# Kernel tuning notes

Measured on AMD Instinct MI355X. Metric: run time of the kernel, lower is better.

The kernel has to match this reference:

```python
import jax, jax.numpy as jnp
import numpy as np

D_MODEL = 1024
NUM_HEAD = 16
HEAD_DIM = D_MODEL // NUM_HEAD  # 64


def setup_inputs() -> dict:
    key = jax.random.key(0)
    ks = jax.random.split(key, 9)
    B, S = 2, 2048
    s = 0.02
    return {
        "x": jax.random.normal(ks[0], (B, S, D_MODEL), dtype=jnp.float32),
        "Wq": jax.random.normal(ks[1], (D_MODEL, D_MODEL), dtype=jnp.float32) * s,
        "bq": jax.random.normal(ks[2], (D_MODEL,), dtype=jnp.float32) * s,
        "Wk": jax.random.normal(ks[3], (D_MODEL, D_MODEL), dtype=jnp.float32) * s,
        "bk": jax.random.normal(ks[4], (D_MODEL,), dtype=jnp.float32) * s,
        "Wv": jax.random.normal(ks[5], (D_MODEL, D_MODEL), dtype=jnp.float32) * s,
        "bv": jax.random.normal(ks[6], (D_MODEL,), dtype=jnp.float32) * s,
        "Wo": jax.random.normal(ks[7], (D_MODEL, D_MODEL), dtype=jnp.float32) * s,
        "bo": jax.random.normal(ks[8], (D_MODEL,), dtype=jnp.float32) * s,
    }


def _split_head(t):
    # [B,S,D] -> [B,H,S,hd]
    B, S, _ = t.shape
    return t.reshape(B, S, NUM_HEAD, HEAD_DIM).transpose(0, 2, 1, 3)


def reference(x, Wq, bq, Wk, bk, Wv, bv, Wo, bo):
    B, S, D = x.shape
    q = _split_head(x @ Wq.T + bq)  # [B,H,S,hd]
    k = _split_head(x @ Wk.T + bk)
    v = _split_head(x @ Wv.T + bv)
    scale = 1.0 / jnp.sqrt(jnp.asarray(HEAD_DIM, dtype=x.dtype))
    scores = jnp.einsum("bhqd,bhkd->bhqk", q, k) * scale  # [B,H,S,S]
    attn = jax.nn.softmax(scores, axis=-1)
    out = jnp.einsum("bhqk,bhkd->bhqd", attn, v)  # [B,H,S,hd]
    out = out.transpose(0, 2, 1, 3).reshape(B, S, D)
    return out @ Wo.T + bo
```

## Files before the change

### kernel.cpp

```cpp
#include <hip/hip_runtime.h>
#include <cstdint>


typedef unsigned short ush;
typedef __bf16 bf16x8 __attribute__((ext_vector_type(8)));
typedef float f32x4 __attribute__((ext_vector_type(4)));
typedef ush u16x8 __attribute__((ext_vector_type(8)));
typedef ush u16x4 __attribute__((ext_vector_type(4)));
typedef unsigned int u32x4 __attribute__((ext_vector_type(4)));

__device__ __forceinline__ ush f2bf(float f) {
  unsigned int u = __float_as_uint(f);
  u += 0x7fffu + ((u >> 16) & 1u);
  return (ush)(u >> 16);
}

__device__ __forceinline__ unsigned int pack2bf_ru(float a, float b) {
  unsigned int ua = __float_as_uint(a) + 0x8000u;
  unsigned int ub = __float_as_uint(b) + 0x8000u;
  return __builtin_amdgcn_perm(ub, ua, 0x07060302u);
}

__device__ __forceinline__ bf16x8 bc8(u16x8 v) {
  return __builtin_bit_cast(bf16x8, v);
}

__device__ __forceinline__ void async16(const void* g, void* l) {
  __builtin_amdgcn_global_load_lds(
      (const __attribute__((address_space(1))) unsigned int*)(uintptr_t)g,
      (__attribute__((address_space(3))) unsigned int*)(uintptr_t)l, 16, 0, 0);
}

__global__ __launch_bounds__(256) void convert_kernel(
    const float* __restrict__ x, const float* __restrict__ Wq,
    const float* __restrict__ Wk, const float* __restrict__ Wv,
    const float* __restrict__ Wo,
    ush* __restrict__ xb, ush* __restrict__ Wqb, ush* __restrict__ Wkb,
    ush* __restrict__ Wvb, ush* __restrict__ Wob)
{
  int tid = blockIdx.x * 256 + threadIdx.x;
  int base = tid * 4;
  const float* src; ush* dst; int idx;
  if (base < 4194304) { src = x; dst = xb; idx = base; }
  else {
    int r = base - 4194304;
    int seg = r >> 20;
    idx = r & 1048575;
    src = seg == 0 ? Wq : seg == 1 ? Wk : seg == 2 ? Wv : Wo;
    dst = seg == 0 ? Wqb : seg == 1 ? Wkb : seg == 2 ? Wvb : Wob;
  }
  float4 f = *(const float4*)(src + idx);
  u16x4 u = { f2bf(f.x), f2bf(f.y), f2bf(f.z), f2bf(f.w) };
  *(u16x4*)(dst + idx) = u;
}

__device__ __forceinline__ void gemm128_core(
    const ush* __restrict__ gA, const ush* __restrict__ gB,
    int m0, int n0, ush* lA, ush* lB, f32x4 (&acc)[4][4])
{
  const int t = threadIdx.x, w = t >> 6, lane = t & 63;
  const int l15 = lane & 15, quad = lane >> 4;
  const int wm = (w >> 1) * 64, wn = (w & 1) * 64;
#pragma unroll
  for (int i = 0; i < 4; ++i)
#pragma unroll
    for (int j = 0; j < 4; ++j) acc[i][j] = (f32x4){0.f, 0.f, 0.f, 0.f};

  for (int kt = 0; kt < 1024; kt += 64) {
#pragma unroll
    for (int i = 0; i < 4; ++i) {
      int j = i * 256 + w * 64 + lane;
      int row = j >> 3, cc = (j & 7) ^ (row & 7);
      async16(gA + (size_t)(m0 + row) * 1024 + kt + cc * 8,
              lA + (i * 256 + w * 64) * 8);
    }
#pragma unroll
    for (int i = 0; i < 4; ++i) {
      int j = i * 256 + w * 64 + lane;
      int row = j >> 3, cc = (j & 7) ^ (row & 7);
      async16(gB + (size_t)(n0 + row) * 1024 + kt + cc * 8,
              lB + (i * 256 + w * 64) * 8);
    }
    __syncthreads();
#pragma unroll
    for (int kf = 0; kf < 2; ++kf) {
      bf16x8 aF[4], bF[4];
#pragma unroll
      for (int mt = 0; mt < 4; ++mt) {
        int row = wm + mt * 16 + l15;
        aF[mt] = bc8(*(const u16x8*)(lA + row * 64 + (((kf * 4 + quad) ^ (row & 7)) * 8)));
      }
#pragma unroll
      for (int nt = 0; nt < 4; ++nt) {
        int row = wn + nt * 16 + l15;
        bF[nt] = bc8(*(const u16x8*)(lB + row * 64 + (((kf * 4 + quad) ^ (row & 7)) * 8)));
      }
#pragma unroll
      for (int mt = 0; mt < 4; ++mt)
#pragma unroll
        for (int nt = 0; nt < 4; ++nt)
          acc[mt][nt] = __builtin_amdgcn_mfma_f32_16x16x32_bf16(
              aF[mt], bF[nt], acc[mt][nt], 0, 0, 0);
    }
    __syncthreads();
  }
}

__global__ __launch_bounds__(256, 2) void qkv_gemm(
    const ush* __restrict__ xb, const ush* __restrict__ Wqb,
    const ush* __restrict__ Wkb, const ush* __restrict__ Wvb,
    const float* __restrict__ bq, const float* __restrict__ bk,
    const float* __restrict__ bv,
    ush* __restrict__ q, ush* __restrict__ k, ush* __restrict__ vt)
{
  int bid = blockIdx.x;
  int wsel = bid >> 8;
  int rem = bid & 255;
  int m0 = (rem & 31) * 128;
  int n0 = (rem >> 5) * 128;
  const ush* gB = wsel == 0 ? Wqb : wsel == 1 ? Wkb : Wvb;
  const float* bias = wsel == 0 ? bq : wsel == 1 ? bk : bv;
  const float oscale = wsel == 1 ? 0.180336880f : 1.0f;

  __shared__ alignas(16) ush lA[128 * 64];
  __shared__ alignas(16) ush lB[128 * 64];
  f32x4 acc[4][4];
  gemm128_core(xb, gB, m0, n0, lA, lB, acc);

  const int t = threadIdx.x, w = t >> 6, lane = t & 63;
  const int l15 = lane & 15, quad = lane >> 4;
  const int wm = (w >> 1) * 64, wn = (w & 1) * 64;
  if (wsel == 2) {
#pragma unroll
    for (int nt = 0; nt < 4; ++nt) {
      int o = n0 + wn + nt * 16 + l15;
      float bl = bias[o];
      int h = o >> 6, d = o & 63;
#pragma unroll
      for (int mt = 0; mt < 4; ++mt) {
        int tb = m0 + wm + mt * 16 + quad * 4;
        int b = tb >> 11, s = tb & 2047;
        int so = s & 63;
        int sp = (s & ~63) | (so & 35) | ((so & 12) << 1) | ((so & 16) >> 2);
        u16x4 pk = { f2bf(acc[mt][nt][0] + bl), f2bf(acc[mt][nt][1] + bl),
                     f2bf(acc[mt][nt][2] + bl), f2bf(acc[mt][nt][3] + bl) };
        *(u16x4*)(vt + (size_t)(((b * 16 + h) * 64) + d) * 2048 + sp) = pk;
      }
    }
  } else {
    ush* dst = wsel == 0 ? q : k;
#pragma unroll
    for (int nt = 0; nt < 4; ++nt) {
      int o = n0 + wn + nt * 16 + l15;
      float bl = bias[o];
      int h = o >> 6, d = o & 63;
#pragma unroll
      for (int mt = 0; mt < 4; ++mt)
#pragma unroll
        for (int r = 0; r < 4; ++r) {
          int token = m0 + wm + mt * 16 + quad * 4 + r;
          int b = token >> 11, s = token & 2047;
          dst[(size_t)(((b * 16 + h) * 2048) + s) * 64 + d] =
              f2bf((acc[mt][nt][r] + bl) * oscale);
        }
    }
  }
}

__global__ __launch_bounds__(128, 2) void attn_kernel(
    const ush* __restrict__ Q, const ush* __restrict__ K,
    const ush* __restrict__ VT, ush* __restrict__ O)
{
  const int bid = blockIdx.x;
  const int bh = (bid & 7) * 4 + (bid >> 8);
  const int qt = (bid >> 3) & 31;
  const ush* qb = Q + (size_t)bh * 2048 * 64;
  const ush* kb = K + (size_t)bh * 2048 * 64;
  const ush* vtb = VT + (size_t)bh * 64 * 2048;
  const int t = threadIdx.x, w = t >> 6, lane = t & 63;
  const int l15 = lane & 15, quad = lane >> 4;
  const int q0 = qt * 64;

  __shared__ alignas(16) ush lK[2][64 * 64];
  __shared__ alignas(16) ush lV[2][64 * 64];

  const int r0 = t >> 3;
  const int c0 = (t & 7) ^ (r0 & 7);
  const ush* kSrc = kb + (size_t)r0 * 64 + c0 * 8;
  const ush* vSrc = vtb + (size_t)r0 * 2048 + c0 * 8;

  bf16x8 qF[4][2];
#pragma unroll
  for (int g = 0; g < 4; ++g)
#pragma unroll
    for (int kf = 0; kf < 2; ++kf)
      qF[g][kf] = bc8(*(const u16x8*)(qb + (size_t)(q0 + g * 16 + l15) * 64 +
                                      kf * 32 + quad * 8));

  float li[4] = {0.f, 0.f, 0.f, 0.f};
  f32x4 accO[4][4];
#pragma unroll
  for (int g = 0; g < 4; ++g)
#pragma unroll
    for (int dt = 0; dt < 4; ++dt) accO[g][dt] = (f32x4){0.f, 0.f, 0.f, 0.f};

#pragma unroll
  for (int i = 0; i < 4; ++i) {
    async16(kSrc + i * 1024, lK[0] + (i * 128 + t) * 8);
    async16(vSrc + (size_t)i * 16 * 2048, lV[0] + (i * 128 + t) * 8);
  }
  __syncthreads();

  for (int it = 0; it < 32; ++it) {
    const int cur = it & 1, nxt = cur ^ 1;
    if (it + 1 < 32) {
      const size_t ko = (size_t)(it + 1) * 64 * 64;
      const int vo = (it + 1) * 64;
#pragma unroll
      for (int i = 0; i < 4; ++i) {
        async16(kSrc + ko + i * 1024, lK[nxt] + (i * 128 + t) * 8);
        async16(vSrc + vo + (size_t)i * 16 * 2048, lV[nxt] + (i * 128 + t) * 8);
      }
    }
    const ush* lk = lK[cur];
    const ush* lv = lV[cur];

    f32x4 sc[4][2];
#pragma unroll
    for (int g = 0; g < 4; ++g)
#pragma unroll
      for (int mt = 0; mt < 2; ++mt) sc[g][mt] = (f32x4){0.f, 0.f, 0.f, 0.f};
#pragma unroll
    for (int kf = 0; kf < 2; ++kf) {
#pragma unroll
      for (int mt = 0; mt < 2; ++mt) {
        int row = (2 * w + mt) * 16 + l15;
        bf16x8 aK = bc8(*(const u16x8*)(lk + row * 64 + (((kf * 4 + quad) ^ (row & 7)) * 8)));
#pragma unroll
        for (int g = 0; g < 4; ++g)
          sc[g][mt] = __builtin_amdgcn_mfma_f32_16x16x32_bf16(
              aK, qF[g][kf], sc[g][mt], 0, 0, 0);
      }
    }

#pragma unroll
    for (int g = 0; g < 4; ++g) {
      float rs = 0.f;
#pragma unroll
      for (int mt = 0; mt < 2; ++mt)
#pragma unroll
        for (int r = 0; r < 4; ++r) {
          sc[g][mt][r] = __builtin_amdgcn_exp2f(sc[g][mt][r]);
          rs += sc[g][mt][r];
        }
      rs += __shfl_xor(rs, 16);
      rs += __shfl_xor(rs, 32);
      li[g] += rs;
    }

    bf16x8 aV[4];
#pragma unroll
    for (int dt = 0; dt < 4; ++dt)
      aV[dt] = bc8(*(const u16x8*)(lv + (dt * 16 + l15) * 64 +
                                   (((w * 4 + quad) ^ (l15 & 7)) * 8)));
#pragma unroll
    for (int g = 0; g < 4; ++g) {
      u32x4 bw = { pack2bf_ru(sc[g][0][0], sc[g][0][1]),
                   pack2bf_ru(sc[g][0][2], sc[g][0][3]),
                   pack2bf_ru(sc[g][1][0], sc[g][1][1]),
                   pack2bf_ru(sc[g][1][2], sc[g][1][3]) };
      bf16x8 bP = __builtin_bit_cast(bf16x8, bw);
#pragma unroll
      for (int dt = 0; dt < 4; ++dt)
        accO[g][dt] = __builtin_amdgcn_mfma_f32_16x16x32_bf16(
            aV[dt], bP, accO[g][dt], 0, 0, 0);
    }
    __syncthreads();
  }

  float* redO = (float*)lK;
  float* redL = (float*)lV;
#define SEND_GROUP(G)                                                        \
  {                                                                          \
    _Pragma("unroll")                                                        \
    for (int dt = 0; dt < 4; ++dt)                                           \
      *(f32x4*)(redO + (((G) * 4 + dt) * 64 + lane) * 4) = accO[G][dt];      \
    redL[(G) * 64 + lane] = li[G];                                           \
  }
  if (w == 0) { SEND_GROUP(2); SEND_GROUP(3); }
  else        { SEND_GROUP(0); SEND_GROUP(1); }
  __syncthreads();
  const int b = bh >> 4, h = bh & 15;
#define FINISH_GROUP(G)                                                      \
  {                                                                          \
    _Pragma("unroll")                                                        \
    for (int dt = 0; dt < 4; ++dt)                                           \
      accO[G][dt] += *(const f32x4*)(redO + (((G) * 4 + dt) * 64 + lane) * 4);\
    float lsum = li[G] + redL[(G) * 64 + lane];                              \
    const float linv = __builtin_amdgcn_rcpf(lsum);                          \
    const int s = q0 + (G) * 16 + l15;                                       \
    _Pragma("unroll")                                                        \
    for (int dt = 0; dt < 4; ++dt) {                                         \
      u16x4 pk = { f2bf(accO[G][dt][0] * linv), f2bf(accO[G][dt][1] * linv), \
                   f2bf(accO[G][dt][2] * linv), f2bf(accO[G][dt][3] * linv) };\
      *(u16x4*)(O + (size_t)(b * 2048 + s) * 1024 + h * 64 + dt * 16 +       \
                quad * 4) = pk;                                              \
    }                                                                        \
  }
  if (w == 0) { FINISH_GROUP(0); FINISH_GROUP(1); }
  else        { FINISH_GROUP(2); FINISH_GROUP(3); }
#undef SEND_GROUP
#undef FINISH_GROUP
}

__global__ __launch_bounds__(256, 2) void out_gemm(
    const ush* __restrict__ ab, const ush* __restrict__ Wob,
    const float* __restrict__ bo, float* __restrict__ out)
{
  int rem = blockIdx.x;
  int m0 = (rem & 31) * 128;
  int n0 = (rem >> 5) * 128;
  __shared__ alignas(16) ush lA[128 * 64];
  __shared__ alignas(16) ush lB[128 * 64];
  f32x4 acc[4][4];
  gemm128_core(ab, Wob, m0, n0, lA, lB, acc);

  const int t = threadIdx.x, w = t >> 6, lane = t & 63;
  const int l15 = lane & 15, quad = lane >> 4;
  const int wm = (w >> 1) * 64, wn = (w & 1) * 64;
#pragma unroll
  for (int nt = 0; nt < 4; ++nt) {
    int o = n0 + wn + nt * 16 + l15;
    float bl = bo[o];
#pragma unroll
    for (int mt = 0; mt < 4; ++mt)
#pragma unroll
      for (int r = 0; r < 4; ++r) {
        int token = m0 + wm + mt * 16 + quad * 4 + r;
        out[(size_t)token * 1024 + o] = acc[mt][nt][r] + bl;
      }
  }
}

extern "C" void kernel_launch(void* const* d_in, const int* in_sizes, int n_in,
                              void* d_out, int out_size, void* d_ws, size_t ws_size,
                              hipStream_t stream)
{
  const float* x  = (const float*)d_in[0];
  const float* Wq = (const float*)d_in[1];
  const float* bq = (const float*)d_in[2];
  const float* Wk = (const float*)d_in[3];
  const float* bk = (const float*)d_in[4];
  const float* Wv = (const float*)d_in[5];
  const float* bv = (const float*)d_in[6];
  const float* Wo = (const float*)d_in[7];
  const float* bo = (const float*)d_in[8];
  float* out = (float*)d_out;

  char* ws = (char*)d_ws;
  ush* xb  = (ush*)(ws);
  ush* Wqb = (ush*)(ws + (size_t)( 8u << 20));
  ush* Wkb = (ush*)(ws + (size_t)(10u << 20));
  ush* Wvb = (ush*)(ws + (size_t)(12u << 20));
  ush* Wob = (ush*)(ws + (size_t)(14u << 20));
  ush* qb  = (ush*)(ws + (size_t)(16u << 20));
  ush* kb  = (ush*)(ws + (size_t)(24u << 20));
  ush* vtb = (ush*)(ws + (size_t)(32u << 20));
  ush* ab  = (ush*)(ws + (size_t)(40u << 20));

  convert_kernel<<<8192, 256, 0, stream>>>(x, Wq, Wk, Wv, Wo,
                                           xb, Wqb, Wkb, Wvb, Wob);
  qkv_gemm<<<768, 256, 0, stream>>>(xb, Wqb, Wkb, Wvb, bq, bk, bv, qb, kb, vtb);
  attn_kernel<<<1024, 128, 0, stream>>>(qb, kb, vtb, ab);
  out_gemm<<<256, 256, 0, stream>>>(ab, Wob, bo, out);
}
```

Baseline: 186.1 us.

## Partition K/V LDS tiles per wave and replace block barriers with waitcnt

Each of the two waves now loads only the K rows and V columns it consumes into its own private LDS slices, so the per-iteration __syncthreads can be dropped in favour of a vmcnt wait. All LDS fragment reads for the current tile are hoisted ahead of issuing the next tile's async loads, which keeps the double buffer safe without a block barrier. The goal is to remove the cross-wave synchronisation stalls in the attention loop. The risk is that the correctness of the per-wave ordering now rests on the hardcoded waitcnt encoding and the sched barriers.

```diff
diff --git a/kernel.cpp b/kernel.cpp
--- a/kernel.cpp
+++ b/kernel.cpp
@@ -181,13 +181,12 @@
   const int l15 = lane & 15, quad = lane >> 4;
   const int q0 = qt * 64;
 
-  __shared__ alignas(16) ush lK[2][64 * 64];
-  __shared__ alignas(16) ush lV[2][64 * 64];
-
-  const int r0 = t >> 3;
-  const int c0 = (t & 7) ^ (r0 & 7);
-  const ush* kSrc = kb + (size_t)r0 * 64 + c0 * 8;
-  const ush* vSrc = vtb + (size_t)r0 * 2048 + c0 * 8;
+  __shared__ alignas(16) ush lK[2][2][32 * 64];
+  __shared__ alignas(16) ush lV[2][2][64 * 32];
+  const int kOff = (lane & 7) ^ ((lane >> 3) & 7);
+  const int cV = ((lane & 3) ^ ((lane >> 2) & 3)) + 4 * w;
+  const ush* kSrcW = kb + (size_t)(32 * w + (lane >> 3)) * 64 + kOff * 8;
+  const ush* vSrcW = vtb + (size_t)(lane >> 2) * 2048 + cV * 8;
 
   bf16x8 qF[4][2];
 #pragma unroll
@@ -206,24 +205,42 @@
 
 #pragma unroll
   for (int i = 0; i < 4; ++i) {
-    async16(kSrc + i * 1024, lK[0] + (i * 128 + t) * 8);
-    async16(vSrc + (size_t)i * 16 * 2048, lV[0] + (i * 128 + t) * 8);
-  }
-  __syncthreads();
+    async16(kSrcW + i * 512, &lK[0][w][0] + (i * 64 + lane) * 8);
+    async16(vSrcW + (size_t)i * 16 * 2048, &lV[0][w][0] + (i * 64 + lane) * 8);
+  }
 
   for (int it = 0; it < 32; ++it) {
     const int cur = it & 1, nxt = cur ^ 1;
+    __builtin_amdgcn_s_waitcnt(0x0F70);
+    __builtin_amdgcn_sched_barrier(0);
+    const ush* lk = &lK[cur][w][0];
+    const ush* lv = &lV[cur][w][0];
+
+    bf16x8 aK[2][2], aV[4];
+#pragma unroll
+    for (int kf = 0; kf < 2; ++kf)
+#pragma unroll
+      for (int mt = 0; mt < 2; ++mt) {
+        int lr = mt * 16 + l15;
+        aK[kf][mt] = bc8(*(const u16x8*)(lk + lr * 64 +
+                                         (((kf * 4 + quad) ^ (lr & 7)) * 8)));
+      }
+#pragma unroll
+    for (int dt = 0; dt < 4; ++dt)
+      aV[dt] = bc8(*(const u16x8*)(lv + (dt * 16 + l15) * 32 +
+                                   ((quad ^ (l15 & 3)) * 8)));
+    __builtin_amdgcn_sched_barrier(0);
+
     if (it + 1 < 32) {
-      const size_t ko = (size_t)(it + 1) * 64 * 64;
+      const size_t ko = (size_t)(it + 1) * 4096;
       const int vo = (it + 1) * 64;
 #pragma unroll
       for (int i = 0; i < 4; ++i) {
-        async16(kSrc + ko + i * 1024, lK[nxt] + (i * 128 + t) * 8);
-        async16(vSrc + vo + (size_t)i * 16 * 2048, lV[nxt] + (i * 128 + t) * 8);
-      }
-    }
-    const ush* lk = lK[cur];
-    const ush* lv = lV[cur];
+        async16(kSrcW + ko + i * 512, &lK[nxt][w][0] + (i * 64 + lane) * 8);
+        async16(vSrcW + vo + (size_t)i * 16 * 2048,
+                &lV[nxt][w][0] + (i * 64 + lane) * 8);
+      }
+    }
 
     f32x4 sc[4][2];
 #pragma unroll
@@ -231,17 +248,13 @@
 #pragma unroll
       for (int mt = 0; mt < 2; ++mt) sc[g][mt] = (f32x4){0.f, 0.f, 0.f, 0.f};
 #pragma unroll
-    for (int kf = 0; kf < 2; ++kf) {
-#pragma unroll
-      for (int mt = 0; mt < 2; ++mt) {
-        int row = (2 * w + mt) * 16 + l15;
-        bf16x8 aK = bc8(*(const u16x8*)(lk + row * 64 + (((kf * 4 + quad) ^ (row & 7)) * 8)));
+    for (int kf = 0; kf < 2; ++kf)
+#pragma unroll
+      for (int mt = 0; mt < 2; ++mt)
 #pragma unroll
         for (int g = 0; g < 4; ++g)
           sc[g][mt] = __builtin_amdgcn_mfma_f32_16x16x32_bf16(
-              aK, qF[g][kf], sc[g][mt], 0, 0, 0);
-      }
-    }
+              aK[kf][mt], qF[g][kf], sc[g][mt], 0, 0, 0);
 
 #pragma unroll
     for (int g = 0; g < 4; ++g) {
@@ -258,11 +271,6 @@
       li[g] += rs;
     }
 
-    bf16x8 aV[4];
-#pragma unroll
-    for (int dt = 0; dt < 4; ++dt)
-      aV[dt] = bc8(*(const u16x8*)(lv + (dt * 16 + l15) * 64 +
-                                   (((w * 4 + quad) ^ (l15 & 7)) * 8)));
 #pragma unroll
     for (int g = 0; g < 4; ++g) {
       u32x4 bw = { pack2bf_ru(sc[g][0][0], sc[g][0][1]),
@@ -275,8 +283,9 @@
         accO[g][dt] = __builtin_amdgcn_mfma_f32_16x16x32_bf16(
             aV[dt], bP, accO[g][dt], 0, 0, 0);
     }
-    __syncthreads();
-  }
+  }
+
+  __syncthreads();
 
   float* redO = (float*)lK;
   float* redL = (float*)lV;
```

New measurement: 186.5 us. No clear change (+0.2%).
